# Kernel tuning notes

Hardware: AMD Instinct MI355X
Metric: run time of the kernel (lower is better)

Reference implementation:

```python
import jax, jax.numpy as jnp
import numpy as np

FEAT_STRIDE = 32  # 520 // 16
POOL = 7          # adaptive_avg_pool2d target (7,7)
C = 8             # channels consumed as (2 classes x 4 coords)


def setup_inputs() -> dict:
    key = jax.random.key(0)
    k1, k2, k3 = jax.random.split(key, 3)
    H = W = 1024
    conv_out = jax.random.normal(k1, (1, C, H, W), dtype=jnp.float32)
    n = 8192
    # sample pixel-space coords in [0, H*FEAT_STRIDE) and sort so min<=max per axis
    ys = jnp.sort(jax.random.randint(k2, (n, 2), 0, H * FEAT_STRIDE), axis=1)
    xs = jnp.sort(jax.random.randint(k3, (n, 2), 0, W * FEAT_STRIDE), axis=1)
    rois = jnp.stack([ys[:, 0], xs[:, 0], ys[:, 1], xs[:, 1]], axis=1).astype(jnp.int64)
    return {"conv_out": conv_out, "rois": rois}


def _adaptive_bounds(start, length):
    # PyTorch adaptive_avg_pool2d bin edges over [start, start+length)
    j = jnp.arange(POOL)
    lo = start + (j * length) // POOL
    hi = start + ((j + 1) * length + POOL - 1) // POOL  # ceil div
    return lo, hi


def _forward(conv_out, rois):
    r = rois // FEAT_STRIDE
    x = conv_out[0]  # [C, H, W]
    # summed-area table, padded so sat[:, y, x] = sum over [0:y, 0:x)
    sat = jnp.pad(jnp.cumsum(jnp.cumsum(x, axis=1), axis=2),
                  ((0, 0), (1, 0), (1, 0)))  # [C, H+1, W+1]

    def pool_one(roi):
        ymin, xmin = roi[0], roi[1]
        ymax, xmax = roi[2] + 1, roi[3] + 1  # exclusive ends
        ylo, yhi = _adaptive_bounds(ymin, ymax - ymin)
        xlo, xhi = _adaptive_bounds(xmin, xmax - xmin)
        # 7x7 bin sums via inclusion-exclusion on SAT -> [C,7,7]
        s = (sat[:, yhi[:, None], xhi[None, :]]
             - sat[:, ylo[:, None], xhi[None, :]]
             - sat[:, yhi[:, None], xlo[None, :]]
             + sat[:, ylo[:, None], xlo[None, :]])
        area = ((yhi - ylo)[:, None] * (xhi - xlo)[None, :]).astype(s.dtype)
        block7 = s / area                       # adaptive_avg_pool2d -> (7,7)
        return block7.mean(axis=(1, 2))         # adaptive_avg_pool2d -> (1,1), [C]

    pooled = jax.vmap(pool_one)(r)              # [n, C]
    return pooled.reshape(-1, 2, 4)


def reference(conv_out, rois):
    return _forward(conv_out, rois)
```

## Files before the change

### kernel.cpp

```cpp
#include <hip/hip_runtime.h>
#include <cstddef>
#include <cstdint>

#define SATW 1025
#define W8   8200
#define NCH  8
#define NCHUNK 64
#define RR   16

#define SAT_BYTES ((size_t)SATW * W8 * 4)
#define PART_OFF  ((SAT_BYTES + 255) & ~(size_t)255)

__global__ __launch_bounds__(256) void rowscan_kernel(const float* __restrict__ in,
                                                      float* __restrict__ sat) {
    const int y    = blockIdx.x;
    const int t    = threadIdx.x;
    const int lane = t & 63;
    const int wv   = t >> 6;

    __shared__ float lds[NCH][1024];

    for (int k = 0; k < 2; ++k) {
        const int c = wv * 2 + k;
        const float4* r4 = (const float4*)(in + ((size_t)c * 1024 + y) * 1024);
        double chunkbase = 0.0;
#pragma unroll
        for (int j = 0; j < 4; ++j) {
            float4 a = r4[lane + 64 * j];
            double v0 = a.x, v1 = a.y, v2 = a.z, v3 = a.w;
            double s = v0 + v1 + v2 + v3;
            double ps = s;
#pragma unroll
            for (int off = 1; off < 64; off <<= 1) {
                double n = __shfl_up(ps, off, 64);
                if (lane >= off) ps += n;
            }
            double base = chunkbase + ps - s;
            double p0 = base + v0, p1 = p0 + v1, p2 = p1 + v2, p3 = p2 + v3;
            ((float4*)lds[c])[lane + 64 * j] =
                make_float4((float)p0, (float)p1, (float)p2, (float)p3);
            chunkbase += __shfl(ps, 63, 64);
        }
    }
    __syncthreads();

    float* orow = sat + (size_t)(y + 1) * W8;
    for (int f4 = t; f4 < W8 / 4; f4 += 256) {
        int f = f4 * 4;
        float4 o;
        float* po = (float*)&o;
#pragma unroll
        for (int j = 0; j < 4; ++j) {
            int ff = f + j;
            int x = ff >> 3, c = ff & 7;
            po[j] = x ? lds[c][x - 1] : 0.0f;
        }
        ((float4*)orow)[f4] = o;
    }
}

__global__ void colsum_kernel(const float* __restrict__ sat,
                              double* __restrict__ partial) {
    int f  = blockIdx.x * 256 + threadIdx.x;
    int ch = blockIdx.y;
    if (f >= W8) return;
    const float* p = sat + ((size_t)(1 + ch * RR)) * W8 + f;
    double s = 0.0;
#pragma unroll 4
    for (int i = 0; i < RR; ++i) s += (double)p[(size_t)i * W8];
    partial[(size_t)ch * W8 + f] = s;
}

__global__ __launch_bounds__(256) void scanpartial_wave(double* __restrict__ partial) {
    int col  = (blockIdx.x * blockDim.x + threadIdx.x) >> 6;
    int lane = threadIdx.x & 63;
    if (col >= W8) return;
    double v = partial[(size_t)lane * W8 + col];
    double ps = v;
#pragma unroll
    for (int off = 1; off < 64; off <<= 1) {
        double n = __shfl_up(ps, off, 64);
        if (lane >= off) ps += n;
    }
    partial[(size_t)lane * W8 + col] = ps - v;
}

__global__ void colscan_kernel(float* __restrict__ sat,
                               const double* __restrict__ partial) {
    int f  = blockIdx.x * 256 + threadIdx.x;
    int ch = blockIdx.y;
    if (f >= W8) return;
    double run = partial[(size_t)ch * W8 + f];
    if (ch == 0) sat[f] = 0.0f;
    float* p = sat + ((size_t)(1 + ch * RR)) * W8 + f;
#pragma unroll 4
    for (int i = 0; i < RR; ++i) {
        run += (double)p[(size_t)i * W8];
        p[(size_t)i * W8] = (float)run;
    }
}

__global__ __launch_bounds__(256) void pool_kernel(const float* __restrict__ sat,
                                                   const int* __restrict__ rois,
                                                   float* __restrict__ out,
                                                   int n_roi) {
    int lane = threadIdx.x & 63;
    int roi  = (blockIdx.x * blockDim.x + threadIdx.x) >> 6;
    if (roi >= n_roi) return;

    const int4 rv = ((const int4*)rois)[roi];
    int ymin = rv.x >> 5;
    int xmin = rv.y >> 5;
    int Ly   = (rv.z >> 5) + 1 - ymin;
    int Lx   = (rv.w >> 5) + 1 - xmin;

    double acc[NCH];
#pragma unroll
    for (int c = 0; c < NCH; ++c) acc[c] = 0.0;

    if (lane < 49) {
        int by = lane / 7;
        int bx = lane - by * 7;
        int ylo = ymin + (by * Ly) / 7;
        int yhi = ymin + ((by + 1) * Ly + 6) / 7;
        int xlo = xmin + (bx * Lx) / 7;
        int xhi = xmin + ((bx + 1) * Lx + 6) / 7;
        double inv = 1.0 / (double)((yhi - ylo) * (xhi - xlo));

        float4 a[2], b[2], c4[2], d[2];
        const float4* hh = (const float4*)(sat + ((size_t)yhi * SATW + xhi) * NCH);
        const float4* lh = (const float4*)(sat + ((size_t)ylo * SATW + xhi) * NCH);
        const float4* hl = (const float4*)(sat + ((size_t)yhi * SATW + xlo) * NCH);
        const float4* ll = (const float4*)(sat + ((size_t)ylo * SATW + xlo) * NCH);
        a[0] = hh[0]; a[1] = hh[1];
        b[0] = lh[0]; b[1] = lh[1];
        c4[0] = hl[0]; c4[1] = hl[1];
        d[0] = ll[0]; d[1] = ll[1];
        const float* fa = (const float*)a;
        const float* fb = (const float*)b;
        const float* fc = (const float*)c4;
        const float* fd = (const float*)d;
#pragma unroll
        for (int c = 0; c < NCH; ++c) {
            double v = (double)fa[c] - (double)fb[c] - (double)fc[c] + (double)fd[c];
            acc[c] = v * inv;
        }
    }

#pragma unroll
    for (int off = 32; off; off >>= 1) {
#pragma unroll
        for (int c = 0; c < NCH; ++c) acc[c] += __shfl_down(acc[c], off, 64);
    }

    if (lane == 0) {
        float4* po = (float4*)(out + (size_t)roi * NCH);
        po[0] = make_float4((float)(acc[0] * (1.0 / 49.0)),
                            (float)(acc[1] * (1.0 / 49.0)),
                            (float)(acc[2] * (1.0 / 49.0)),
                            (float)(acc[3] * (1.0 / 49.0)));
        po[1] = make_float4((float)(acc[4] * (1.0 / 49.0)),
                            (float)(acc[5] * (1.0 / 49.0)),
                            (float)(acc[6] * (1.0 / 49.0)),
                            (float)(acc[7] * (1.0 / 49.0)));
    }
}

extern "C" void kernel_launch(void* const* d_in, const int* in_sizes, int n_in,
                              void* d_out, int out_size, void* d_ws, size_t ws_size,
                              hipStream_t stream) {
    const float* conv = (const float*)d_in[0];
    const int*   rois = (const int*)d_in[1];
    float*       out  = (float*)d_out;
    int n_roi = in_sizes[1] / 4;

    float*  sat     = (float*)d_ws;
    double* partial = (double*)((char*)d_ws + PART_OFF);

    rowscan_kernel<<<1024, 256, 0, stream>>>(conv, sat);
    colsum_kernel<<<dim3(33, NCHUNK), 256, 0, stream>>>(sat, partial);
    scanpartial_wave<<<(W8 * 64 + 255) / 256, 256, 0, stream>>>(partial);
    colscan_kernel<<<dim3(33, NCHUNK), 256, 0, stream>>>(sat, partial);
    pool_kernel<<<(n_roi + 3) / 4, 256, 0, stream>>>(sat, rois, out, n_roi);
}
```

Baseline: 124.5 us.

## Fuse column scan into single-pass wave kernel and use float in pooling

Replaces the three-kernel column scan (chunk sums, scan of partials, rescan) with one kernel. In it, each 64-lane wave owns 32 columns and walks down all rows 8 at a time, carrying a running double-precision prefix through shuffles. This removes one full read pass over the SAT and the partial buffer. The pooling kernel also switches its inclusion-exclusion and reduction from double to float. The risk is low parallelism: only about 257 single-wave blocks each run 128 serial iterations with a one-step prefetch, which may starve memory bandwidth.

```diff
diff --git a/kernel.cpp b/kernel.cpp
--- a/kernel.cpp
+++ b/kernel.cpp
@@ -5,11 +5,6 @@
 #define SATW 1025
 #define W8   8200
 #define NCH  8
-#define NCHUNK 64
-#define RR   16
-
-#define SAT_BYTES ((size_t)SATW * W8 * 4)
-#define PART_OFF  ((SAT_BYTES + 255) & ~(size_t)255)
 
 __global__ __launch_bounds__(256) void rowscan_kernel(const float* __restrict__ in,
                                                       float* __restrict__ sat) {
@@ -59,44 +54,43 @@
     }
 }
 
-__global__ void colsum_kernel(const float* __restrict__ sat,
-                              double* __restrict__ partial) {
-    int f  = blockIdx.x * 256 + threadIdx.x;
-    int ch = blockIdx.y;
-    if (f >= W8) return;
-    const float* p = sat + ((size_t)(1 + ch * RR)) * W8 + f;
-    double s = 0.0;
-#pragma unroll 4
-    for (int i = 0; i < RR; ++i) s += (double)p[(size_t)i * W8];
-    partial[(size_t)ch * W8 + f] = s;
-}
+__global__ __launch_bounds__(64) void colscan_fused(float* __restrict__ sat) {
+    const int lane = threadIdx.x;
+    const int r    = lane >> 3;
+    const int q    = lane & 7;
+    const int c0   = blockIdx.x * 32 + q * 4;
+    const bool act = (c0 + 3) < W8;
 
-__global__ __launch_bounds__(256) void scanpartial_wave(double* __restrict__ partial) {
-    int col  = (blockIdx.x * blockDim.x + threadIdx.x) >> 6;
-    int lane = threadIdx.x & 63;
-    if (col >= W8) return;
-    double v = partial[(size_t)lane * W8 + col];
-    double ps = v;
+    if (r == 0 && act)
+        *(float4*)(sat + c0) = make_float4(0.f, 0.f, 0.f, 0.f);
+
+    double cd0 = 0, cd1 = 0, cd2 = 0, cd3 = 0;
+    float* p = sat + (size_t)(1 + r) * W8 + c0;
+
+    float4 v = act ? *(const float4*)p : make_float4(0.f, 0.f, 0.f, 0.f);
+    for (int it = 0; it < 128; ++it) {
+        float4 vn = make_float4(0.f, 0.f, 0.f, 0.f);
+        if (it < 127 && act) vn = *(const float4*)(p + 8 * W8);
+
+        double d0 = v.x, d1 = v.y, d2 = v.z, d3 = v.w;
 #pragma unroll
-    for (int off = 1; off < 64; off <<= 1) {
-        double n = __shfl_up(ps, off, 64);
-        if (lane >= off) ps += n;
-    }
-    partial[(size_t)lane * W8 + col] = ps - v;
-}
+        for (int s = 8; s <= 32; s <<= 1) {
+            double t0 = __shfl_up(d0, s, 64);
+            double t1 = __shfl_up(d1, s, 64);
+            double t2 = __shfl_up(d2, s, 64);
+            double t3 = __shfl_up(d3, s, 64);
+            if (lane >= s) { d0 += t0; d1 += t1; d2 += t2; d3 += t3; }
+        }
+        if (act)
+            *(float4*)p = make_float4((float)(cd0 + d0), (float)(cd1 + d1),
+                                      (float)(cd2 + d2), (float)(cd3 + d3));
+        cd0 += __shfl(d0, 56 + q, 64);
+        cd1 += __shfl(d1, 56 + q, 64);
+        cd2 += __shfl(d2, 56 + q, 64);
+        cd3 += __shfl(d3, 56 + q, 64);
 
-__global__ void colscan_kernel(float* __restrict__ sat,
-                               const double* __restrict__ partial) {
-    int f  = blockIdx.x * 256 + threadIdx.x;
-    int ch = blockIdx.y;
-    if (f >= W8) return;
-    double run = partial[(size_t)ch * W8 + f];
-    if (ch == 0) sat[f] = 0.0f;
-    float* p = sat + ((size_t)(1 + ch * RR)) * W8 + f;
-#pragma unroll 4
-    for (int i = 0; i < RR; ++i) {
-        run += (double)p[(size_t)i * W8];
-        p[(size_t)i * W8] = (float)run;
+        p += 8 * W8;
+        v = vn;
     }
 }
 
@@ -114,9 +108,9 @@
     int Ly   = (rv.z >> 5) + 1 - ymin;
     int Lx   = (rv.w >> 5) + 1 - xmin;
 
-    double acc[NCH];
+    float acc[NCH];
 #pragma unroll
-    for (int c = 0; c < NCH; ++c) acc[c] = 0.0;
+    for (int c = 0; c < NCH; ++c) acc[c] = 0.0f;
 
     if (lane < 49) {
         int by = lane / 7;
@@ -125,7 +119,7 @@
         int yhi = ymin + ((by + 1) * Ly + 6) / 7;
         int xlo = xmin + (bx * Lx) / 7;
         int xhi = xmin + ((bx + 1) * Lx + 6) / 7;
-        double inv = 1.0 / (double)((yhi - ylo) * (xhi - xlo));
+        float inv = 1.0f / (float)((yhi - ylo) * (xhi - xlo));
 
         float4 a[2], b[2], c4[2], d[2];
         const float4* hh = (const float4*)(sat + ((size_t)yhi * SATW + xhi) * NCH);
@@ -141,10 +135,8 @@
         const float* fc = (const float*)c4;
         const float* fd = (const float*)d;
 #pragma unroll
-        for (int c = 0; c < NCH; ++c) {
-            double v = (double)fa[c] - (double)fb[c] - (double)fc[c] + (double)fd[c];
-            acc[c] = v * inv;
-        }
+        for (int c = 0; c < NCH; ++c)
+            acc[c] = (fa[c] - fb[c] - fc[c] + fd[c]) * inv;
     }
 
 #pragma unroll
@@ -154,15 +146,10 @@
     }
 
     if (lane == 0) {
+        const float k = 1.0f / 49.0f;
         float4* po = (float4*)(out + (size_t)roi * NCH);
-        po[0] = make_float4((float)(acc[0] * (1.0 / 49.0)),
-                            (float)(acc[1] * (1.0 / 49.0)),
-                            (float)(acc[2] * (1.0 / 49.0)),
-                            (float)(acc[3] * (1.0 / 49.0)));
-        po[1] = make_float4((float)(acc[4] * (1.0 / 49.0)),
-                            (float)(acc[5] * (1.0 / 49.0)),
-                            (float)(acc[6] * (1.0 / 49.0)),
-                            (float)(acc[7] * (1.0 / 49.0)));
+        po[0] = make_float4(acc[0] * k, acc[1] * k, acc[2] * k, acc[3] * k);
+        po[1] = make_float4(acc[4] * k, acc[5] * k, acc[6] * k, acc[7] * k);
     }
 }
 
@@ -174,12 +161,9 @@
     float*       out  = (float*)d_out;
     int n_roi = in_sizes[1] / 4;
 
-    float*  sat     = (float*)d_ws;
-    double* partial = (double*)((char*)d_ws + PART_OFF);
+    float* sat = (float*)d_ws;
 
     rowscan_kernel<<<1024, 256, 0, stream>>>(conv, sat);
-    colsum_kernel<<<dim3(33, NCHUNK), 256, 0, stream>>>(sat, partial);
-    scanpartial_wave<<<(W8 * 64 + 255) / 256, 256, 0, stream>>>(partial);
-    colscan_kernel<<<dim3(33, NCHUNK), 256, 0, stream>>>(sat, partial);
+    colscan_fused<<<(W8 + 31) / 32, 64, 0, stream>>>(sat);
     pool_kernel<<<(n_roi + 3) / 4, 256, 0, stream>>>(sat, rois, out, n_roi);
 }
```

After: 175.3 us. 40.8% more time.
